# Performance work log

Hardware: AMD Instinct MI355X
Metric: run time of the kernel (lower is better)

The kernel has to match this reference:

```python
import jax, jax.numpy as jnp
import numpy as np

NUM_CLASS = 31
B = 4096
F_IN = 2048
F_BOT = 256


def setup_inputs() -> dict:
    key = jax.random.key(0)
    ks = jax.random.split(key, 6)
    return {
        "source": jax.random.normal(ks[0], (B, F_IN), dtype=jnp.float32),
        "target": jax.random.normal(ks[1], (B, F_IN), dtype=jnp.float32),
        "W_b": jax.random.normal(ks[2], (F_IN, F_BOT), dtype=jnp.float32) * (1.0 / np.sqrt(F_IN)),
        "b_b": jnp.zeros((F_BOT,), dtype=jnp.float32),
        "W_c": jax.random.normal(ks[3], (F_BOT, NUM_CLASS), dtype=jnp.float32) * (1.0 / np.sqrt(F_BOT)),
        "b_c": jnp.zeros((NUM_CLASS,), dtype=jnp.float32),
        "source_label": jax.random.randint(ks[4], (B,), 0, NUM_CLASS, dtype=jnp.int64),
    }


def _conf_margin(logits, labels):
    # get_confidence_output_margin: softmax confidence margin vs best wrong class
    conf = jax.nn.softmax(logits, axis=-1)
    mask = jax.nn.one_hot(labels, NUM_CLASS, dtype=conf.dtype)
    targets_conf = jnp.sum(conf * mask, axis=1)
    max_excl_conf = jnp.max(conf * (1.0 - mask), axis=1)
    return targets_conf - max_excl_conf


def _pairwise_sqdist(s, t):
    # ||x_p - x_q||^2 computed as a single GEMM + broadcast (replaces python double loop)
    s2 = jnp.sum(s * s, axis=1)  # [Bs]
    t2 = jnp.sum(t * t, axis=1)  # [Bt]
    d2 = s2[:, None] + t2[None, :] - 2.0 * (s @ t.T)
    return jnp.maximum(d2, 0.0)


def reference(source, target, W_b, b_b, W_c, b_c, source_label):
    # bottleneck: Linear + ReLU (shared weights for both domains)
    src = jax.nn.relu(source @ W_b + b_b)  # [B, 256]
    tar = jax.nn.relu(target @ W_b + b_b)  # [B, 256]

    src_clf = src @ W_c + b_c  # [B, 31]
    tar_clf = tar @ W_c + b_c  # [B, 31]

    # cross entropy on source
    logp = jax.nn.log_softmax(src_clf, axis=-1)
    clf_loss = -jnp.mean(jnp.take_along_axis(logp, source_label[:, None], axis=1))

    src_margin = _conf_margin(src_clf, source_label)
    tar_margin = _conf_margin(tar_clf, jnp.argmax(tar_clf, axis=1))

    # no_grad diagnostics: MMD + Gaussian kernel means (amplitude=1, sigma in {1,5})
    delta = jnp.mean(src, axis=0) - jnp.mean(tar, axis=0)
    curr_mmd = jax.lax.stop_gradient(delta @ delta)
    d2 = _pairwise_sqdist(src, tar)  # [B, B]
    curr_gk1 = jax.lax.stop_gradient(jnp.mean(jnp.exp(-0.5 * d2)))
    curr_gk5 = jax.lax.stop_gradient(jnp.mean(jnp.exp(-d2 / 50.0)))

    return jnp.concatenate([
        jnp.stack([clf_loss, curr_mmd, curr_gk1, curr_gk5]),
        src_margin,
        tar_margin,
    ])  # [4 + 2B]
```

## Files before the change

### kernel.cpp

```cpp
#include <hip/hip_runtime.h>
#include <stdint.h>

#define DI __device__ __forceinline__

typedef float f32x4 __attribute__((ext_vector_type(4)));
typedef short bf16x8 __attribute__((ext_vector_type(8)));

DI uint16_t f2bf(float f) {
    union { float f; uint32_t u; } v; v.f = f;
    uint32_t r = v.u + 0x7FFF + ((v.u >> 16) & 1);
    return (uint16_t)(r >> 16);
}
DI float bf2f(uint16_t h) {
    union { uint32_t u; float f; } v; v.u = ((uint32_t)h) << 16;
    return v.f;
}
DI void gl_lds16(const void* g, void* l) {
    __builtin_amdgcn_global_load_lds(
        (__attribute__((address_space(1))) void*)(uintptr_t)g,
        (__attribute__((address_space(3))) void*)(uintptr_t)l,
        16, 0, 0);
}

__global__ void k_init(const float* __restrict__ Wc, uint16_t* __restrict__ WcT,
                       float* __restrict__ accs) {
    int tid = threadIdx.x;
    if (tid < 4) accs[tid] = 0.f;
    for (int idx = tid; idx < 32 * 256; idx += 256) {
        int n = idx >> 8, k = idx & 255;
        WcT[idx] = (n < 31) ? f2bf(Wc[k * 31 + n]) : (uint16_t)0;
    }
}

__global__ void k_transpose_wb(const float* __restrict__ Wb, uint16_t* __restrict__ WbT) {
    __shared__ float t[32][33];
    int kb = blockIdx.x, nb = blockIdx.y;
    int tx = threadIdx.x & 31, ty0 = (threadIdx.x >> 5) * 4;
    for (int i = 0; i < 4; ++i)
        t[ty0 + i][tx] = Wb[(kb * 32 + ty0 + i) * 256 + nb * 32 + tx];
    __syncthreads();
    for (int i = 0; i < 4; ++i)
        WbT[(nb * 32 + ty0 + i) * 2048 + kb * 32 + tx] = f2bf(t[tx][ty0 + i]);
}

__launch_bounds__(256)
__global__ void k_bottleneck(const float* __restrict__ src, const float* __restrict__ tgt,
                             const uint16_t* __restrict__ WbT, const float* __restrict__ bb,
                             uint16_t* __restrict__ Y) {
    __shared__ __align__(16) uint8_t lds[20480];
    int tid = threadIdx.x;
    int lane = tid & 63, w = tid >> 6;
    int bm = blockIdx.x >> 1, bn = blockIdx.x & 1;
    int m0 = bm * 32;
    const float* X = (m0 < 4096) ? (src + (size_t)m0 * 2048)
                                 : (tgt + (size_t)(m0 - 4096) * 2048);
    int ar = tid >> 3, akb = (tid >> 2) & 1, ap = tid & 3;
    int ac = ap ^ (ar & 3) ^ ((ar >> 2) & 3);
    const float* Ag = X + ar * 2048 + akb * 32 + ac * 8;
    uint8_t* Aw = lds + akb * 2048 + ar * 64 + ap * 16;
    int cc = (lane >> 4) ^ (lane & 3) ^ ((lane >> 2) & 3);
    f32x4 acc[2][2] = {};
    for (int t = 0; t < 32; ++t) {
        int k0 = t * 64;
        if (t) __syncthreads();
        for (int i = 0; i < 4; ++i) {
            int s = w * 4 + i;
            int kb = s >> 3, r0 = (s & 7) * 16;
            int r = r0 + (lane >> 2), p = lane & 3;
            int c = p ^ (r & 3) ^ ((r >> 2) & 3);
            gl_lds16(WbT + (size_t)(bn * 128 + r) * 2048 + k0 + kb * 32 + c * 8,
                     lds + 4096 + s * 1024);
        }
        float4 x0 = *(const float4*)(Ag + k0);
        float4 x1 = *(const float4*)(Ag + k0 + 4);
        uint4 u;
        u.x = (uint32_t)f2bf(x0.x) | ((uint32_t)f2bf(x0.y) << 16);
        u.y = (uint32_t)f2bf(x0.z) | ((uint32_t)f2bf(x0.w) << 16);
        u.z = (uint32_t)f2bf(x1.x) | ((uint32_t)f2bf(x1.y) << 16);
        u.w = (uint32_t)f2bf(x1.z) | ((uint32_t)f2bf(x1.w) << 16);
        *(uint4*)Aw = u;
        __syncthreads();
        for (int kb = 0; kb < 2; ++kb) {
            bf16x8 a[2], b[2];
            for (int mi = 0; mi < 2; ++mi) {
                int r = mi * 16 + (lane & 15);
                a[mi] = *(const bf16x8*)(lds + kb * 2048 + r * 64 + cc * 16);
            }
            for (int nf = 0; nf < 2; ++nf) {
                int rn = w * 32 + nf * 16 + (lane & 15);
                b[nf] = *(const bf16x8*)(lds + 4096 + kb * 8192 + rn * 64 + cc * 16);
            }
            for (int mi = 0; mi < 2; ++mi)
                for (int nf = 0; nf < 2; ++nf)
                    acc[mi][nf] = __builtin_amdgcn_mfma_f32_16x16x32_bf16(
                        a[mi], b[nf], acc[mi][nf], 0, 0, 0);
        }
    }
    for (int mi = 0; mi < 2; ++mi)
        for (int nf = 0; nf < 2; ++nf) {
            int col = bn * 128 + w * 32 + nf * 16 + (lane & 15);
            float bias = bb[col];
            for (int j = 0; j < 4; ++j) {
                int row = m0 + mi * 16 + (lane >> 4) * 4 + j;
                float v = acc[mi][nf][j] + bias;
                v = fmaxf(v, 0.f);
                Y[(size_t)row * 256 + col] = f2bf(v);
            }
        }
}

__global__ void k_rowstats(const uint16_t* __restrict__ Y, float* __restrict__ s2t2) {
    int row = blockIdx.x * 4 + (threadIdx.x >> 6);
    int lane = threadIdx.x & 63;
    ushort4 v = *(const ushort4*)(Y + (size_t)row * 256 + lane * 4);
    float a = bf2f(v.x), b = bf2f(v.y), c = bf2f(v.z), d = bf2f(v.w);
    float s = a * a + b * b + c * c + d * d;
    for (int m = 1; m < 64; m <<= 1) s += __shfl_xor(s, m);
    if (lane == 0) s2t2[row] = s;
}

__global__ void k_colsum(const uint16_t* __restrict__ Y, float* __restrict__ part) {
    int c = threadIdx.x;
    int r0 = blockIdx.x * 64;
    float acc = 0.f;
    for (int r = r0; r < r0 + 64; ++r) acc += bf2f(Y[(size_t)r * 256 + c]);
    part[blockIdx.x * 256 + c] = acc;
}

__launch_bounds__(256)
__global__ void k_classifier(const uint16_t* __restrict__ Y, const uint16_t* __restrict__ WcT,
                             const float* __restrict__ bc, const int* __restrict__ labels,
                             float* __restrict__ out_margin, float* __restrict__ ce_acc) {
    __shared__ __align__(16) uint8_t lds[49152];
    int tid = threadIdx.x, lane = tid & 63, w = tid >> 6;
    int m0 = blockIdx.x * 64;
    int cc = (lane >> 4) ^ (lane & 3) ^ ((lane >> 2) & 3);
    for (int s = w; s < 48; s += 4) {
        int r, p, c;
        if (s < 32) {
            int kb = s >> 2, r0 = (s & 3) * 16;
            r = r0 + (lane >> 2); p = lane & 3;
            c = p ^ (r & 3) ^ ((r >> 2) & 3);
            gl_lds16(Y + (size_t)(m0 + r) * 256 + kb * 32 + c * 8, lds + s * 1024);
        } else {
            int s2 = s - 32;
            int kb = s2 >> 1, r0 = (s2 & 1) * 16;
            r = r0 + (lane >> 2); p = lane & 3;
            c = p ^ (r & 3) ^ ((r >> 2) & 3);
            gl_lds16(WcT + r * 256 + kb * 32 + c * 8, lds + 32768 + s2 * 1024);
        }
    }
    __syncthreads();
    f32x4 acc[2] = {};
    for (int kb = 0; kb < 8; ++kb) {
        int r = w * 16 + (lane & 15);
        bf16x8 a = *(const bf16x8*)(lds + kb * 4096 + r * 64 + cc * 16);
        for (int nf = 0; nf < 2; ++nf) {
            int rn = nf * 16 + (lane & 15);
            bf16x8 b = *(const bf16x8*)(lds + 32768 + kb * 2048 + rn * 64 + cc * 16);
            acc[nf] = __builtin_amdgcn_mfma_f32_16x16x32_bf16(a, b, acc[nf], 0, 0, 0);
        }
    }
    int c0 = lane & 15, c1 = 16 + c0;
    float bc0 = bc[c0];
    float bc1 = (c1 < 31) ? bc[c1] : 0.f;
    bool is_src = (m0 < 4096);
    float ce_local = 0.f;
    for (int j = 0; j < 4; ++j) {
        int row = m0 + w * 16 + (lane >> 4) * 4 + j;
        float v0 = acc[0][j] + bc0;
        float v1 = (c1 < 31) ? (acc[1][j] + bc1) : -1e30f;
        float mx = fmaxf(v0, v1);
        for (int m = 1; m < 16; m <<= 1) mx = fmaxf(mx, __shfl_xor(mx, m, 16));
        float e0 = __expf(v0 - mx);
        float e1 = (c1 < 31) ? __expf(v1 - mx) : 0.f;
        float ssum = e0 + e1;
        for (int m = 1; m < 16; m <<= 1) ssum += __shfl_xor(ssum, m, 16);
        float inv = 1.f / ssum;
        float conf0 = e0 * inv, conf1 = e1 * inv;
        int lab;
        if (is_src) {
            lab = labels[row];
        } else {
            float bv; int bi;
            if (v0 >= v1) { bv = v0; bi = c0; } else { bv = v1; bi = c1; }
            for (int m = 1; m < 16; m <<= 1) {
                float ov = __shfl_xor(bv, m, 16);
                int oi = __shfl_xor(bi, m, 16);
                if (ov > bv || (ov == bv && oi < bi)) { bv = ov; bi = oi; }
            }
            lab = bi;
        }
        float tc = (c0 == lab ? conf0 : 0.f) + (c1 == lab ? conf1 : 0.f);
        for (int m = 1; m < 16; m <<= 1) tc += __shfl_xor(tc, m, 16);
        float ex = fmaxf(c0 == lab ? -1.f : conf0,
                         (c1 == lab || c1 >= 31) ? -1.f : conf1);
        for (int m = 1; m < 16; m <<= 1) ex = fmaxf(ex, __shfl_xor(ex, m, 16));
        if (c0 == 0) out_margin[row] = tc - ex;
        if (is_src) {
            float vl = (c0 == lab) ? v0 : ((c1 == lab) ? v1 : -1e30f);
            for (int m = 1; m < 16; m <<= 1) vl = fmaxf(vl, __shfl_xor(vl, m, 16));
            if (c0 == 0) ce_local += -(vl - mx - __logf(ssum));
        }
    }
    if (is_src) {
        ce_local += __shfl_xor(ce_local, 16);
        ce_local += __shfl_xor(ce_local, 32);
        if (lane == 0) atomicAdd(ce_acc, ce_local);
    }
}

__launch_bounds__(256)
__global__ void k_pairwise(const uint16_t* __restrict__ Y, const float* __restrict__ s2t2,
                           float* __restrict__ gk_part) {
    __shared__ __align__(16) uint8_t lds[65536];
    int tid = threadIdx.x, lane = tid & 63, w = tid >> 6;
    int m0 = blockIdx.x * 128, n0 = blockIdx.y * 128;
    int cc = (lane >> 4) ^ (lane & 3) ^ ((lane >> 2) & 3);
    int wm = (w & 1) * 64, wn = (w >> 1) * 64;
    f32x4 acc[4][4] = {};
    for (int h = 0; h < 2; ++h) {
        if (h) __syncthreads();
        int k0 = h * 128;
        for (int i = 0; i < 8; ++i) {
            int s = w * 8 + i;
            int kb = s >> 3, r0 = (s & 7) * 16;
            int r = r0 + (lane >> 2), p = lane & 3;
            int c = p ^ (r & 3) ^ ((r >> 2) & 3);
            gl_lds16(Y + (size_t)(m0 + r) * 256 + k0 + kb * 32 + c * 8, lds + s * 1024);
            gl_lds16(Y + (size_t)(4096 + n0 + r) * 256 + k0 + kb * 32 + c * 8,
                     lds + 32768 + s * 1024);
        }
        __syncthreads();
        for (int kb = 0; kb < 4; ++kb) {
            bf16x8 a[4], b[4];
            for (int mi = 0; mi < 4; ++mi) {
                int r = wm + mi * 16 + (lane & 15);
                a[mi] = *(const bf16x8*)(lds + kb * 8192 + r * 64 + cc * 16);
            }
            for (int nf = 0; nf < 4; ++nf) {
                int rn = wn + nf * 16 + (lane & 15);
                b[nf] = *(const bf16x8*)(lds + 32768 + kb * 8192 + rn * 64 + cc * 16);
            }
            for (int mi = 0; mi < 4; ++mi)
                for (int nf = 0; nf < 4; ++nf)
                    acc[mi][nf] = __builtin_amdgcn_mfma_f32_16x16x32_bf16(
                        a[mi], b[nf], acc[mi][nf], 0, 0, 0);
        }
    }
    float t2v[4];
    for (int nf = 0; nf < 4; ++nf)
        t2v[nf] = s2t2[4096 + n0 + wn + nf * 16 + (lane & 15)];
    float g1 = 0.f, g5 = 0.f;
    for (int mi = 0; mi < 4; ++mi) {
        int rbase = m0 + wm + mi * 16 + (lane >> 4) * 4;
        float s2v[4];
        for (int j = 0; j < 4; ++j) s2v[j] = s2t2[rbase + j];
        for (int nf = 0; nf < 4; ++nf)
            for (int j = 0; j < 4; ++j) {
                float d2 = s2v[j] + t2v[nf] - 2.f * acc[mi][nf][j];
                d2 = fmaxf(d2, 0.f);
                g1 += __expf(-0.5f * d2);
                g5 += __expf(-0.02f * d2);
            }
    }
    for (int m = 1; m < 64; m <<= 1) { g1 += __shfl_xor(g1, m); g5 += __shfl_xor(g5, m); }
    __syncthreads();
    float* red = (float*)lds;
    if (lane == 0) { red[w * 2] = g1; red[w * 2 + 1] = g5; }
    __syncthreads();
    if (tid == 0) {
        int bid = blockIdx.y * 32 + blockIdx.x;
        gk_part[bid * 2]     = red[0] + red[2] + red[4] + red[6];
        gk_part[bid * 2 + 1] = red[1] + red[3] + red[5] + red[7];
    }
}

__global__ void k_finalize(const float* __restrict__ colsum_part,
                           const float* __restrict__ gk_part,
                           const float* __restrict__ accs, float* __restrict__ d_out) {
    __shared__ float red[12];
    int tid = threadIdx.x, lane = tid & 63, w = tid >> 6;
    float cs = 0.f, ct = 0.f;
    for (int b = 0; b < 64; ++b)  cs += colsum_part[b * 256 + tid];
    for (int b = 64; b < 128; ++b) ct += colsum_part[b * 256 + tid];
    float delta = (cs - ct) * (1.f / 4096.f);
    float sq = delta * delta;
    float g1 = 0.f, g5 = 0.f;
    for (int i = 0; i < 4; ++i) {
        int p = tid * 4 + i;
        g1 += gk_part[p * 2];
        g5 += gk_part[p * 2 + 1];
    }
    for (int m = 1; m < 64; m <<= 1) {
        sq += __shfl_xor(sq, m);
        g1 += __shfl_xor(g1, m);
        g5 += __shfl_xor(g5, m);
    }
    if (lane == 0) { red[w * 3] = sq; red[w * 3 + 1] = g1; red[w * 3 + 2] = g5; }
    __syncthreads();
    if (tid == 0) {
        d_out[0] = accs[0] * (1.f / 4096.f);
        d_out[1] = red[0] + red[3] + red[6] + red[9];
        d_out[2] = (red[1] + red[4] + red[7] + red[10]) * 5.9604644775390625e-08f;
        d_out[3] = (red[2] + red[5] + red[8] + red[11]) * 5.9604644775390625e-08f;
    }
}

extern "C" void kernel_launch(void* const* d_in, const int* in_sizes, int n_in,
                              void* d_out, int out_size, void* d_ws, size_t ws_size,
                              hipStream_t stream) {
    const float* source = (const float*)d_in[0];
    const float* target = (const float*)d_in[1];
    const float* Wb     = (const float*)d_in[2];
    const float* bb     = (const float*)d_in[3];
    const float* Wc     = (const float*)d_in[4];
    const float* bc     = (const float*)d_in[5];
    const int*   labels = (const int*)d_in[6];
    float* out = (float*)d_out;
    uint8_t* ws = (uint8_t*)d_ws;

    uint16_t* Y    = (uint16_t*)(ws);
    uint16_t* WbT  = (uint16_t*)(ws + 4194304);
    uint16_t* WcT  = (uint16_t*)(ws + 5242880);
    float*    s2t2 = (float*)(ws + 5259264);
    float*    accs = (float*)(ws + 5292032);
    float*    colsum_part = (float*)(ws + 4194304);
    float*    gk_part     = (float*)(ws + 4194304 + 131072);

    k_init<<<1, 256, 0, stream>>>(Wc, WcT, accs);
    k_transpose_wb<<<dim3(64, 8), 256, 0, stream>>>(Wb, WbT);
    k_bottleneck<<<512, 256, 0, stream>>>(source, target, WbT, bb, Y);
    k_rowstats<<<2048, 256, 0, stream>>>(Y, s2t2);
    k_colsum<<<128, 256, 0, stream>>>(Y, colsum_part);
    k_classifier<<<128, 256, 0, stream>>>(Y, WcT, bc, labels, out + 4, accs);
    k_pairwise<<<dim3(32, 32), 256, 0, stream>>>(Y, s2t2, gk_part);
    k_finalize<<<1, 256, 0, stream>>>(colsum_part, gk_part, accs, out);
}
```

Before: 179.0 us.

## Rework bottleneck GEMM with register prefetch and slim classifier, colsum, pairwise kernels

The bottleneck GEMM drops LDS staging and barriers. Each wave now loads its fp32 A rows and bf16 B fragments straight into registers, prefetching A two iterations ahead and B one ahead, with 64x64 output tiles. The classifier becomes one-wave blocks that read operands directly from global memory, and it writes per-block cross-entropy partials that the finalize kernel sums instead of using an atomic. Colsum switches to vectorized loads with an LDS reduction, and pairwise uses smaller 64-wide K stages so its LDS footprint is halved. The risks are weaker B reuse across waves, since it now relies only on cache, and higher register pressure in the bottleneck.

Result: slower. 219.0 us (+22.3%).

```diff
diff --git a/kernel.cpp b/kernel.cpp
--- a/kernel.cpp
+++ b/kernel.cpp
@@ -1,4 +1,5 @@
 #include <hip/hip_runtime.h>
+#include <hip/hip_bf16.h>
 #include <stdint.h>
 
 #define DI __device__ __forceinline__
@@ -14,6 +15,10 @@
 DI float bf2f(uint16_t h) {
     union { uint32_t u; float f; } v; v.u = ((uint32_t)h) << 16;
     return v.f;
+}
+DI uint32_t pk_bf16(float x, float y) {
+    __hip_bfloat162 h = __float22bfloat162_rn(make_float2(x, y));
+    union { __hip_bfloat162 h; uint32_t u; } v; v.h = h; return v.u;
 }
 DI void gl_lds16(const void* g, void* l) {
     __builtin_amdgcn_global_load_lds(
@@ -22,10 +27,8 @@
         16, 0, 0);
 }
 
-__global__ void k_init(const float* __restrict__ Wc, uint16_t* __restrict__ WcT,
-                       float* __restrict__ accs) {
+__global__ void k_init(const float* __restrict__ Wc, uint16_t* __restrict__ WcT) {
     int tid = threadIdx.x;
-    if (tid < 4) accs[tid] = 0.f;
     for (int idx = tid; idx < 32 * 256; idx += 256) {
         int n = idx >> 8, k = idx & 255;
         WcT[idx] = (n < 31) ? f2bf(Wc[k * 31 + n]) : (uint16_t)0;
@@ -45,68 +48,68 @@
 
 __launch_bounds__(256)
 __global__ void k_bottleneck(const float* __restrict__ src, const float* __restrict__ tgt,
-                             const uint16_t* __restrict__ WbT, const float* __restrict__ bb,
+                             const uint16_t* __restrict__ WbT, const float* __restrict__ bbias,
                              uint16_t* __restrict__ Y) {
-    __shared__ __align__(16) uint8_t lds[20480];
-    int tid = threadIdx.x;
-    int lane = tid & 63, w = tid >> 6;
-    int bm = blockIdx.x >> 1, bn = blockIdx.x & 1;
-    int m0 = bm * 32;
-    const float* X = (m0 < 4096) ? (src + (size_t)m0 * 2048)
-                                 : (tgt + (size_t)(m0 - 4096) * 2048);
-    int ar = tid >> 3, akb = (tid >> 2) & 1, ap = tid & 3;
-    int ac = ap ^ (ar & 3) ^ ((ar >> 2) & 3);
-    const float* Ag = X + ar * 2048 + akb * 32 + ac * 8;
-    uint8_t* Aw = lds + akb * 2048 + ar * 64 + ap * 16;
-    int cc = (lane >> 4) ^ (lane & 3) ^ ((lane >> 2) & 3);
-    f32x4 acc[2][2] = {};
+    int tid = threadIdx.x, lane = tid & 63, w = tid >> 6;
+    int bm = blockIdx.x >> 2, bn = blockIdx.x & 3;
+    int rowbase = bm * 64 + w * 16;
+    const float* Xr = (rowbase < 4096) ? src + (size_t)rowbase * 2048
+                                       : tgt + (size_t)(rowbase - 4096) * 2048;
+    int rl = lane & 15, kq = lane >> 4;
+    const float* Ab = Xr + (size_t)rl * 2048 + kq * 8;
+    int n0 = bn * 64;
+    const uint16_t* Bb = WbT + (size_t)(n0 + rl) * 2048 + kq * 8;
+
+    f32x4 acc[4] = {};
+    float4 ar[4][4];
+    bf16x8 br[2][2][4];
+
+    auto loadA = [&](int buf, int t) {
+        const float* p = Ab + t * 64;
+        ar[buf][0] = *(const float4*)(p);
+        ar[buf][1] = *(const float4*)(p + 4);
+        ar[buf][2] = *(const float4*)(p + 32);
+        ar[buf][3] = *(const float4*)(p + 36);
+    };
+    auto loadB = [&](int buf, int t) {
+        const uint16_t* p = Bb + t * 64;
+        for (int nf = 0; nf < 4; ++nf) {
+            br[buf][0][nf] = *(const bf16x8*)(p + nf * 16 * 2048);
+            br[buf][1][nf] = *(const bf16x8*)(p + nf * 16 * 2048 + 32);
+        }
+    };
+    loadA(0, 0); loadA(1, 1); loadB(0, 0);
+
+#pragma unroll 4
     for (int t = 0; t < 32; ++t) {
-        int k0 = t * 64;
-        if (t) __syncthreads();
-        for (int i = 0; i < 4; ++i) {
-            int s = w * 4 + i;
-            int kb = s >> 3, r0 = (s & 7) * 16;
-            int r = r0 + (lane >> 2), p = lane & 3;
-            int c = p ^ (r & 3) ^ ((r >> 2) & 3);
-            gl_lds16(WbT + (size_t)(bn * 128 + r) * 2048 + k0 + kb * 32 + c * 8,
-                     lds + 4096 + s * 1024);
-        }
-        float4 x0 = *(const float4*)(Ag + k0);
-        float4 x1 = *(const float4*)(Ag + k0 + 4);
-        uint4 u;
-        u.x = (uint32_t)f2bf(x0.x) | ((uint32_t)f2bf(x0.y) << 16);
-        u.y = (uint32_t)f2bf(x0.z) | ((uint32_t)f2bf(x0.w) << 16);
-        u.z = (uint32_t)f2bf(x1.x) | ((uint32_t)f2bf(x1.y) << 16);
-        u.w = (uint32_t)f2bf(x1.z) | ((uint32_t)f2bf(x1.w) << 16);
-        *(uint4*)Aw = u;
-        __syncthreads();
-        for (int kb = 0; kb < 2; ++kb) {
-            bf16x8 a[2], b[2];
-            for (int mi = 0; mi < 2; ++mi) {
-                int r = mi * 16 + (lane & 15);
-                a[mi] = *(const bf16x8*)(lds + kb * 2048 + r * 64 + cc * 16);
-            }
-            for (int nf = 0; nf < 2; ++nf) {
-                int rn = w * 32 + nf * 16 + (lane & 15);
-                b[nf] = *(const bf16x8*)(lds + 4096 + kb * 8192 + rn * 64 + cc * 16);
-            }
-            for (int mi = 0; mi < 2; ++mi)
-                for (int nf = 0; nf < 2; ++nf)
-                    acc[mi][nf] = __builtin_amdgcn_mfma_f32_16x16x32_bf16(
-                        a[mi], b[nf], acc[mi][nf], 0, 0, 0);
-        }
-    }
-    for (int mi = 0; mi < 2; ++mi)
-        for (int nf = 0; nf < 2; ++nf) {
-            int col = bn * 128 + w * 32 + nf * 16 + (lane & 15);
-            float bias = bb[col];
-            for (int j = 0; j < 4; ++j) {
-                int row = m0 + mi * 16 + (lane >> 4) * 4 + j;
-                float v = acc[mi][nf][j] + bias;
-                v = fmaxf(v, 0.f);
-                Y[(size_t)row * 256 + col] = f2bf(v);
-            }
-        }
+        int abuf = t & 3, bbuf = t & 1;
+        if (t < 30) loadA((t + 2) & 3, t + 2);
+        if (t < 31) loadB(bbuf ^ 1, t + 1);
+        union { uint4 u; bf16x8 v; } a0, a1;
+        a0.u.x = pk_bf16(ar[abuf][0].x, ar[abuf][0].y);
+        a0.u.y = pk_bf16(ar[abuf][0].z, ar[abuf][0].w);
+        a0.u.z = pk_bf16(ar[abuf][1].x, ar[abuf][1].y);
+        a0.u.w = pk_bf16(ar[abuf][1].z, ar[abuf][1].w);
+        a1.u.x = pk_bf16(ar[abuf][2].x, ar[abuf][2].y);
+        a1.u.y = pk_bf16(ar[abuf][2].z, ar[abuf][2].w);
+        a1.u.z = pk_bf16(ar[abuf][3].x, ar[abuf][3].y);
+        a1.u.w = pk_bf16(ar[abuf][3].z, ar[abuf][3].w);
+#pragma unroll
+        for (int nf = 0; nf < 4; ++nf)
+            acc[nf] = __builtin_amdgcn_mfma_f32_16x16x32_bf16(a0.v, br[bbuf][0][nf], acc[nf], 0, 0, 0);
+#pragma unroll
+        for (int nf = 0; nf < 4; ++nf)
+            acc[nf] = __builtin_amdgcn_mfma_f32_16x16x32_bf16(a1.v, br[bbuf][1][nf], acc[nf], 0, 0, 0);
+    }
+    for (int nf = 0; nf < 4; ++nf) {
+        int col = n0 + nf * 16 + rl;
+        float bias = bbias[col];
+        for (int j = 0; j < 4; ++j) {
+            int row = rowbase + kq * 4 + j;
+            float v = fmaxf(acc[nf][j] + bias, 0.f);
+            Y[(size_t)row * 256 + col] = f2bf(v);
+        }
+    }
 }
 
 __global__ void k_rowstats(const uint16_t* __restrict__ Y, float* __restrict__ s2t2) {
@@ -120,54 +123,50 @@
 }
 
 __global__ void k_colsum(const uint16_t* __restrict__ Y, float* __restrict__ part) {
-    int c = threadIdx.x;
+    __shared__ float sred[4][256];
+    int tid = threadIdx.x, cg = tid & 63, rs = tid >> 6;
     int r0 = blockIdx.x * 64;
-    float acc = 0.f;
-    for (int r = r0; r < r0 + 64; ++r) acc += bf2f(Y[(size_t)r * 256 + c]);
-    part[blockIdx.x * 256 + c] = acc;
-}
-
-__launch_bounds__(256)
+    float a0 = 0.f, a1 = 0.f, a2 = 0.f, a3 = 0.f;
+    for (int r = r0 + rs; r < r0 + 64; r += 4) {
+        ushort4 v = *(const ushort4*)(Y + (size_t)r * 256 + cg * 4);
+        a0 += bf2f(v.x); a1 += bf2f(v.y); a2 += bf2f(v.z); a3 += bf2f(v.w);
+    }
+    sred[rs][cg * 4 + 0] = a0; sred[rs][cg * 4 + 1] = a1;
+    sred[rs][cg * 4 + 2] = a2; sred[rs][cg * 4 + 3] = a3;
+    __syncthreads();
+    if (rs == 0)
+        for (int i = 0; i < 4; ++i) {
+            int col = cg * 4 + i;
+            part[blockIdx.x * 256 + col] =
+                sred[0][col] + sred[1][col] + sred[2][col] + sred[3][col];
+        }
+}
+
+__launch_bounds__(64)
 __global__ void k_classifier(const uint16_t* __restrict__ Y, const uint16_t* __restrict__ WcT,
                              const float* __restrict__ bc, const int* __restrict__ labels,
-                             float* __restrict__ out_margin, float* __restrict__ ce_acc) {
-    __shared__ __align__(16) uint8_t lds[49152];
-    int tid = threadIdx.x, lane = tid & 63, w = tid >> 6;
-    int m0 = blockIdx.x * 64;
-    int cc = (lane >> 4) ^ (lane & 3) ^ ((lane >> 2) & 3);
-    for (int s = w; s < 48; s += 4) {
-        int r, p, c;
-        if (s < 32) {
-            int kb = s >> 2, r0 = (s & 3) * 16;
-            r = r0 + (lane >> 2); p = lane & 3;
-            c = p ^ (r & 3) ^ ((r >> 2) & 3);
-            gl_lds16(Y + (size_t)(m0 + r) * 256 + kb * 32 + c * 8, lds + s * 1024);
-        } else {
-            int s2 = s - 32;
-            int kb = s2 >> 1, r0 = (s2 & 1) * 16;
-            r = r0 + (lane >> 2); p = lane & 3;
-            c = p ^ (r & 3) ^ ((r >> 2) & 3);
-            gl_lds16(WcT + r * 256 + kb * 32 + c * 8, lds + 32768 + s2 * 1024);
-        }
-    }
-    __syncthreads();
+                             float* __restrict__ out_margin, float* __restrict__ ce_part) {
+    int lane = threadIdx.x;
+    int r0 = blockIdx.x * 16;
+    bool is_src = (r0 < 4096);
+    int rl = lane & 15, kq = lane >> 4;
+    const uint16_t* Ap = Y + (size_t)(r0 + rl) * 256 + kq * 8;
+    const uint16_t* Bp = WcT + (size_t)rl * 256 + kq * 8;
     f32x4 acc[2] = {};
+#pragma unroll
     for (int kb = 0; kb < 8; ++kb) {
-        int r = w * 16 + (lane & 15);
-        bf16x8 a = *(const bf16x8*)(lds + kb * 4096 + r * 64 + cc * 16);
-        for (int nf = 0; nf < 2; ++nf) {
-            int rn = nf * 16 + (lane & 15);
-            bf16x8 b = *(const bf16x8*)(lds + 32768 + kb * 2048 + rn * 64 + cc * 16);
-            acc[nf] = __builtin_amdgcn_mfma_f32_16x16x32_bf16(a, b, acc[nf], 0, 0, 0);
-        }
-    }
-    int c0 = lane & 15, c1 = 16 + c0;
+        bf16x8 a  = *(const bf16x8*)(Ap + kb * 32);
+        bf16x8 b0 = *(const bf16x8*)(Bp + kb * 32);
+        bf16x8 b1 = *(const bf16x8*)(Bp + 16 * 256 + kb * 32);
+        acc[0] = __builtin_amdgcn_mfma_f32_16x16x32_bf16(a, b0, acc[0], 0, 0, 0);
+        acc[1] = __builtin_amdgcn_mfma_f32_16x16x32_bf16(a, b1, acc[1], 0, 0, 0);
+    }
+    int c0 = rl, c1 = 16 + rl;
     float bc0 = bc[c0];
     float bc1 = (c1 < 31) ? bc[c1] : 0.f;
-    bool is_src = (m0 < 4096);
     float ce_local = 0.f;
     for (int j = 0; j < 4; ++j) {
-        int row = m0 + w * 16 + (lane >> 4) * 4 + j;
+        int row = r0 + kq * 4 + j;
         float v0 = acc[0][j] + bc0;
         float v1 = (c1 < 31) ? (acc[1][j] + bc1) : -1e30f;
         float mx = fmaxf(v0, v1);
@@ -203,36 +202,34 @@
             if (c0 == 0) ce_local += -(vl - mx - __logf(ssum));
         }
     }
-    if (is_src) {
-        ce_local += __shfl_xor(ce_local, 16);
-        ce_local += __shfl_xor(ce_local, 32);
-        if (lane == 0) atomicAdd(ce_acc, ce_local);
-    }
+    ce_local += __shfl_xor(ce_local, 16);
+    ce_local += __shfl_xor(ce_local, 32);
+    if (lane == 0) ce_part[blockIdx.x] = is_src ? ce_local : 0.f;
 }
 
 __launch_bounds__(256)
 __global__ void k_pairwise(const uint16_t* __restrict__ Y, const float* __restrict__ s2t2,
                            float* __restrict__ gk_part) {
-    __shared__ __align__(16) uint8_t lds[65536];
+    __shared__ __align__(16) uint8_t lds[32768];
     int tid = threadIdx.x, lane = tid & 63, w = tid >> 6;
     int m0 = blockIdx.x * 128, n0 = blockIdx.y * 128;
     int cc = (lane >> 4) ^ (lane & 3) ^ ((lane >> 2) & 3);
     int wm = (w & 1) * 64, wn = (w >> 1) * 64;
     f32x4 acc[4][4] = {};
-    for (int h = 0; h < 2; ++h) {
+    for (int h = 0; h < 4; ++h) {
         if (h) __syncthreads();
-        int k0 = h * 128;
-        for (int i = 0; i < 8; ++i) {
-            int s = w * 8 + i;
+        int k0 = h * 64;
+        for (int i = 0; i < 4; ++i) {
+            int s = w * 4 + i;
             int kb = s >> 3, r0 = (s & 7) * 16;
             int r = r0 + (lane >> 2), p = lane & 3;
             int c = p ^ (r & 3) ^ ((r >> 2) & 3);
             gl_lds16(Y + (size_t)(m0 + r) * 256 + k0 + kb * 32 + c * 8, lds + s * 1024);
             gl_lds16(Y + (size_t)(4096 + n0 + r) * 256 + k0 + kb * 32 + c * 8,
-                     lds + 32768 + s * 1024);
+                     lds + 16384 + s * 1024);
         }
         __syncthreads();
-        for (int kb = 0; kb < 4; ++kb) {
+        for (int kb = 0; kb < 2; ++kb) {
             bf16x8 a[4], b[4];
             for (int mi = 0; mi < 4; ++mi) {
                 int r = wm + mi * 16 + (lane & 15);
@@ -240,7 +237,7 @@
             }
             for (int nf = 0; nf < 4; ++nf) {
                 int rn = wn + nf * 16 + (lane & 15);
-                b[nf] = *(const bf16x8*)(lds + 32768 + kb * 8192 + rn * 64 + cc * 16);
+                b[nf] = *(const bf16x8*)(lds + 16384 + kb * 8192 + rn * 64 + cc * 16);
             }
             for (int mi = 0; mi < 4; ++mi)
                 for (int nf = 0; nf < 4; ++nf)
@@ -278,11 +275,11 @@
 
 __global__ void k_finalize(const float* __restrict__ colsum_part,
                            const float* __restrict__ gk_part,
-                           const float* __restrict__ accs, float* __restrict__ d_out) {
-    __shared__ float red[12];
+                           const float* __restrict__ ce_part, float* __restrict__ d_out) {
+    __shared__ float red[4][4];
     int tid = threadIdx.x, lane = tid & 63, w = tid >> 6;
     float cs = 0.f, ct = 0.f;
-    for (int b = 0; b < 64; ++b)  cs += colsum_part[b * 256 + tid];
+    for (int b = 0; b < 64; ++b)   cs += colsum_part[b * 256 + tid];
     for (int b = 64; b < 128; ++b) ct += colsum_part[b * 256 + tid];
     float delta = (cs - ct) * (1.f / 4096.f);
     float sq = delta * delta;
@@ -292,18 +289,20 @@
         g1 += gk_part[p * 2];
         g5 += gk_part[p * 2 + 1];
     }
+    float ce = ce_part[tid] + ce_part[tid + 256];
     for (int m = 1; m < 64; m <<= 1) {
         sq += __shfl_xor(sq, m);
         g1 += __shfl_xor(g1, m);
         g5 += __shfl_xor(g5, m);
-    }
-    if (lane == 0) { red[w * 3] = sq; red[w * 3 + 1] = g1; red[w * 3 + 2] = g5; }
+        ce += __shfl_xor(ce, m);
+    }
+    if (lane == 0) { red[w][0] = sq; red[w][1] = g1; red[w][2] = g5; red[w][3] = ce; }
     __syncthreads();
     if (tid == 0) {
-        d_out[0] = accs[0] * (1.f / 4096.f);
-        d_out[1] = red[0] + red[3] + red[6] + red[9];
-        d_out[2] = (red[1] + red[4] + red[7] + red[10]) * 5.9604644775390625e-08f;
-        d_out[3] = (red[2] + red[5] + red[8] + red[11]) * 5.9604644775390625e-08f;
+        d_out[0] = (red[0][3] + red[1][3] + red[2][3] + red[3][3]) * (1.f / 4096.f);
+        d_out[1] = red[0][0] + red[1][0] + red[2][0] + red[3][0];
+        d_out[2] = (red[0][1] + red[1][1] + red[2][1] + red[3][1]) * 5.9604644775390625e-08f;
+        d_out[3] = (red[0][2] + red[1][2] + red[2][2] + red[3][2]) * 5.9604644775390625e-08f;
     }
 }
 
@@ -324,16 +323,16 @@
     uint16_t* WbT  = (uint16_t*)(ws + 4194304);
     uint16_t* WcT  = (uint16_t*)(ws + 5242880);
     float*    s2t2 = (float*)(ws + 5259264);
-    float*    accs = (float*)(ws + 5292032);
-    float*    colsum_part = (float*)(ws + 4194304);
-    float*    gk_part     = (float*)(ws + 4194304 + 131072);
-
-    k_init<<<1, 256, 0, stream>>>(Wc, WcT, accs);
+    float* colsum_part = (float*)(ws + 4194304);
+    float* gk_part     = (float*)(ws + 4194304 + 131072);
+    float* ce_part     = (float*)(ws + 4194304 + 139264);
+
+    k_init<<<1, 256, 0, stream>>>(Wc, WcT);
     k_transpose_wb<<<dim3(64, 8), 256, 0, stream>>>(Wb, WbT);
     k_bottleneck<<<512, 256, 0, stream>>>(source, target, WbT, bb, Y);
     k_rowstats<<<2048, 256, 0, stream>>>(Y, s2t2);
     k_colsum<<<128, 256, 0, stream>>>(Y, colsum_part);
-    k_classifier<<<128, 256, 0, stream>>>(Y, WcT, bc, labels, out + 4, accs);
+    k_classifier<<<512, 64, 0, stream>>>(Y, WcT, bc, labels, out + 4, ce_part);
     k_pairwise<<<dim3(32, 32), 256, 0, stream>>>(Y, s2t2, gk_part);
-    k_finalize<<<1, 256, 0, stream>>>(colsum_part, gk_part, accs, out);
-}
+    k_finalize<<<1, 256, 0, stream>>>(colsum_part, gk_part, ce_part, out);
+}
```
